# Kernel optimization log

Measured on AMD Instinct MI355X. Metric: run time of the kernel, lower is better.

The kernel has to match this reference:

```python
import jax, jax.numpy as jnp
import numpy as np

NUM_Z = 100   # atomic-number bins hardcoded in the module
G = 512       # number of graphs in the batch (segment count)


def setup_inputs() -> dict:
    key = jax.random.key(0)
    k1, k2, k3 = jax.random.split(key, 3)
    N, D = 50000, 64
    out = jax.random.normal(k1, (N, D), dtype=jnp.float32)
    # atomic numbers in [1, 100], matching the (z-1)*D offset logic
    z_rv = jax.random.randint(k2, (N,), 1, NUM_Z + 1)
    # sorted graph ids in [0, G)
    x_rv_batch = jnp.sort(jax.random.randint(k3, (N,), 0, G))
    return {"out": out, "z_rv": z_rv, "x_rv_batch": x_rv_batch}


def reference(out, z_rv, x_rv_batch):
    # Original math: elem_pool[i, (z_i-1)*D : z_i*D] = out[i] (zeros elsewhere),
    # then global_mean_pool(elem_pool, batch) -> [G, 100*D].
    # Fused form: segment-sum node features into (graph, atomic-number) bins,
    # then divide by per-graph node counts. Identical result, no NxD*100 buffer.
    N, D = out.shape
    keys = x_rv_batch * NUM_Z + (z_rv - 1)                 # [N] combined (graph, bin) id
    sums = jax.ops.segment_sum(out, keys, num_segments=G * NUM_Z)   # [G*100, D]
    counts = jax.ops.segment_sum(jnp.ones((N,), out.dtype), x_rv_batch,
                                 num_segments=G)           # [G] nodes per graph
    pooled = sums.reshape(G, NUM_Z * D) / jnp.maximum(counts, 1.0)[:, None]
    return pooled
```

## Files before the change

### kernel.cpp

```cpp
#include <hip/hip_runtime.h>

#define NUM_Z 100
#define NUM_G 512
#define DIM   64
#define THREADS 1024
#define CHUNK 128

__device__ __forceinline__ int lower_bound_wave(const int* __restrict__ arr, int n,
                                                int target, int lane) {
    int lo = 0, len = n;
    while (len > 0) {
        int step = (len + 63) >> 6;
        int idx  = lo + lane * step;
        int v    = (idx < n) ? arr[idx] : 0x7fffffff;
        unsigned long long m = __ballot(v < target);
        int k = (int)__popcll(m);
        if (k == 0) break;
        int rem = k * step; if (rem > len) rem = len;
        int hi  = lo + rem;
        lo += (k - 1) * step + 1;
        len = hi - lo;
    }
    return lo;
}

__global__ __launch_bounds__(THREADS) void anp_stage_kernel(
    const float4* __restrict__ feat,
    const int*    __restrict__ z,
    const int*    __restrict__ batch,
    float*        __restrict__ pooled,
    int n)
{
    __shared__ float4 tile[CHUNK * 16];
    __shared__ int hist[128];
    __shared__ int scan_tmp[128];
    __shared__ int pref[NUM_Z + 1];
    __shared__ int cursor[NUM_Z];
    __shared__ unsigned short idx_sorted[CHUNK];
    __shared__ int sb[2];
    __shared__ int wtot;

    const int g    = blockIdx.x;
    const int tid  = threadIdx.x;
    const int wave = tid >> 6;
    const int lane = tid & 63;
    const int grp  = tid >> 4;
    const int q    = tid & 15;
    const int b0   = 2 * grp;

    if (tid < 128) hist[tid] = 0;
    if (wave < 2) {
        int r = lower_bound_wave(batch, n, g + wave, lane);
        if (lane == 0) sb[wave] = r;
    }
    __syncthreads();
    const int start = sb[0];
    const int end   = sb[1];
    const int cnt   = end - start;

    float4 a0 = make_float4(0.f, 0.f, 0.f, 0.f);
    float4 a1 = make_float4(0.f, 0.f, 0.f, 0.f);

    const int jrow = tid >> 4;

    for (int cs = start; cs < end; cs += CHUNK) {
        const int m = min(CHUNK, end - cs);

        float4 s0, s1;
        const bool h0 = (jrow      < m);
        const bool h1 = (jrow + 64 < m);
        if (h0) s0 = feat[(size_t)(cs + jrow)      * 16 + q];
        if (h1) s1 = feat[(size_t)(cs + jrow + 64) * 16 + q];

        int zv = 0;
        if (tid < m) {
            zv = z[cs + tid] - 1;
            atomicAdd(&hist[zv], 1);
        }
        __syncthreads();

        if (wave < 2) {
            int e = hist[(wave << 6) + lane];
            #pragma unroll
            for (int d = 1; d < 64; d <<= 1) {
                int t = __shfl_up(e, d, 64);
                if (lane >= d) e += t;
            }
            scan_tmp[(wave << 6) + lane] = e;
            if (wave == 0 && lane == 63) wtot = e;
        }
        __syncthreads();

        if (tid <= NUM_Z) {
            int v = (tid == 0) ? 0
                  : scan_tmp[tid - 1] + ((tid - 1) >= 64 ? wtot : 0);
            pref[tid] = v;
            if (tid < NUM_Z) cursor[tid] = v;
        }
        __syncthreads();

        if (h0) tile[jrow * 16 + q]        = s0;
        if (h1) tile[(jrow + 64) * 16 + q] = s1;
        if (tid < m) {
            int p = atomicAdd(&cursor[zv], 1);
            idx_sorted[p] = (unsigned short)(tid | ((zv & 1) << 15));
        }
        __syncthreads();

        if (grp < 50) {
            const int off = pref[b0];
            const int c   = pref[b0 + 2] - off;
            for (int base = 0; base < c; base += 16) {
                const int nb = min(16, c - base);
                int myraw = (q < nb) ? (int)idx_sorted[off + base + q] : 0;
                #pragma unroll 4
                for (int j = 0; j < nb; ++j) {
                    int raw  = __shfl(myraw, ((lane >> 4) << 4) + j, 64);
                    int nd   = raw & 0x7fff;
                    float pm = (float)(raw >> 15);
                    float4 v = tile[nd * 16 + q];
                    float m0 = 1.0f - pm;
                    a0.x = fmaf(v.x, m0, a0.x); a0.y = fmaf(v.y, m0, a0.y);
                    a0.z = fmaf(v.z, m0, a0.z); a0.w = fmaf(v.w, m0, a0.w);
                    a1.x = fmaf(v.x, pm, a1.x); a1.y = fmaf(v.y, pm, a1.y);
                    a1.z = fmaf(v.z, pm, a1.z); a1.w = fmaf(v.w, pm, a1.w);
                }
            }
        }
        if (cs + CHUNK < end) {
            __syncthreads();
            if (tid < 128) hist[tid] = 0;
            __syncthreads();
        }
    }

    if (grp < 50) {
        const float s = 1.0f / (float)(cnt > 1 ? cnt : 1);
        float4* outv = (float4*)(pooled + (size_t)g * (NUM_Z * DIM));
        outv[(b0 + 0) * 16 + q] = make_float4(a0.x*s, a0.y*s, a0.z*s, a0.w*s);
        outv[(b0 + 1) * 16 + q] = make_float4(a1.x*s, a1.y*s, a1.z*s, a1.w*s);
    }
}

extern "C" void kernel_launch(void* const* d_in, const int* in_sizes, int n_in,
                              void* d_out, int out_size, void* d_ws, size_t ws_size,
                              hipStream_t stream) {
    const float* feat  = (const float*)d_in[0];
    const int*   z     = (const int*)d_in[1];
    const int*   batch = (const int*)d_in[2];
    float* pooled = (float*)d_out;
    const int n = in_sizes[0] / DIM;

    anp_stage_kernel<<<NUM_G, THREADS, 0, stream>>>(
        (const float4*)feat, z, batch, pooled, n);
}
```

Baseline: 11.33 us.

## Locate segment bounds via guessed window scan, prefetch z, merge scan stages

Each block guesses a 2048-element window around its expected segment position, loads batch ids and z values for that window in one coalesced pass, and finds segment start/end with ballot-popcount counts instead of a serial binary search over global memory. If the window does not cover the whole segment, it falls back to the old wave binary search. z values are then read from shared memory, and the two-wave histogram scan collapses into one wave, removing a barrier per chunk. The cost is extra global reads of the window for every block and a dependence on segments being roughly uniform in size.

```diff
diff --git a/kernel.cpp b/kernel.cpp
--- a/kernel.cpp
+++ b/kernel.cpp
@@ -5,6 +5,7 @@
 #define DIM   64
 #define THREADS 1024
 #define CHUNK 128
+#define WIN 2048
 
 __device__ __forceinline__ int lower_bound_wave(const int* __restrict__ arr, int n,
                                                 int target, int lane) {
@@ -24,7 +25,7 @@
     return lo;
 }
 
-__global__ __launch_bounds__(THREADS) void anp_stage_kernel(
+__global__ __launch_bounds__(THREADS) void anp_win_kernel(
     const float4* __restrict__ feat,
     const int*    __restrict__ z,
     const int*    __restrict__ batch,
@@ -32,13 +33,14 @@
     int n)
 {
     __shared__ float4 tile[CHUNK * 16];
+    __shared__ int zwin[WIN];
     __shared__ int hist[128];
-    __shared__ int scan_tmp[128];
     __shared__ int pref[NUM_Z + 1];
     __shared__ int cursor[NUM_Z];
     __shared__ unsigned short idx_sorted[CHUNK];
+    __shared__ int Lpart[16], Epart[16];
+    __shared__ int sbf, sbl;
     __shared__ int sb[2];
-    __shared__ int wtot;
 
     const int g    = blockIdx.x;
     const int tid  = threadIdx.x;
@@ -48,19 +50,55 @@
     const int q    = tid & 15;
     const int b0   = 2 * grp;
 
+    int wbase = (int)(((long long)g * n) / NUM_G) - 960;
+    int wmax  = n - WIN; if (wmax < 0) wmax = 0;
+    if (wbase < 0) wbase = 0;
+    if (wbase > wmax) wbase = wmax;
+
+    const int i0 = wbase + tid, i1 = wbase + tid + THREADS;
+    int bv0 = (i0 < n) ? batch[i0] : 0x7fffffff;
+    int bv1 = (i1 < n) ? batch[i1] : 0x7fffffff;
+    int zv0 = (i0 < n) ? z[i0] : 1;
+    int zv1 = (i1 < n) ? z[i1] : 1;
+
     if (tid < 128) hist[tid] = 0;
-    if (wave < 2) {
-        int r = lower_bound_wave(batch, n, g + wave, lane);
-        if (lane == 0) sb[wave] = r;
+    zwin[tid]           = zv0 - 1;
+    zwin[tid + THREADS] = zv1 - 1;
+    {
+        int l = __popcll(__ballot(bv0 < g))     + __popcll(__ballot(bv1 < g));
+        int e = __popcll(__ballot(bv0 < g + 1)) + __popcll(__ballot(bv1 < g + 1));
+        if (lane == 0) { Lpart[wave] = l; Epart[wave] = e; }
     }
+    if (tid == 0)           sbf = bv0;
+    if (tid == THREADS - 1) sbl = bv1;
     __syncthreads();
-    const int start = sb[0];
-    const int end   = sb[1];
-    const int cnt   = end - start;
+
+    int v = 0;
+    if (lane < 16)      v = Lpart[lane];
+    else if (lane < 32) v = Epart[lane - 16];
+    v += __shfl_xor(v, 1, 64); v += __shfl_xor(v, 2, 64);
+    v += __shfl_xor(v, 4, 64); v += __shfl_xor(v, 8, 64);
+    const int L = __shfl(v, 0, 64);
+    const int E = __shfl(v, 16, 64);
+
+    const bool valid = ((wbase == 0) || (sbf < g)) &&
+                       ((wbase + WIN >= n) || (sbl > g));
+    int start, end;
+    if (valid) {
+        start = wbase + L; end = wbase + E;
+    } else {
+        if (wave < 2) {
+            int r = lower_bound_wave(batch, n, g + wave, lane);
+            if (lane == 0) sb[wave] = r;
+        }
+        __syncthreads();
+        start = sb[0]; end = sb[1];
+    }
+    const int cnt = end - start;
+    const int dlt = start - wbase;
 
     float4 a0 = make_float4(0.f, 0.f, 0.f, 0.f);
     float4 a1 = make_float4(0.f, 0.f, 0.f, 0.f);
-
     const int jrow = tid >> 4;
 
     for (int cs = start; cs < end; cs += CHUNK) {
@@ -72,38 +110,36 @@
         if (h0) s0 = feat[(size_t)(cs + jrow)      * 16 + q];
         if (h1) s1 = feat[(size_t)(cs + jrow + 64) * 16 + q];
 
-        int zv = 0;
+        int zb = 0;
         if (tid < m) {
-            zv = z[cs + tid] - 1;
-            atomicAdd(&hist[zv], 1);
+            zb = valid ? zwin[dlt + (cs - start) + tid] : (z[cs + tid] - 1);
+            atomicAdd(&hist[zb], 1);
         }
         __syncthreads();
 
-        if (wave < 2) {
-            int e = hist[(wave << 6) + lane];
+        if (wave == 0) {
+            int h0v = hist[lane], h1v = hist[64 + lane];
+            int i0v = h0v, i1v = h1v;
             #pragma unroll
             for (int d = 1; d < 64; d <<= 1) {
-                int t = __shfl_up(e, d, 64);
-                if (lane >= d) e += t;
+                int t0 = __shfl_up(i0v, d, 64);
+                int t1 = __shfl_up(i1v, d, 64);
+                if (lane >= d) { i0v += t0; i1v += t1; }
             }
-            scan_tmp[(wave << 6) + lane] = e;
-            if (wave == 0 && lane == 63) wtot = e;
-        }
-        __syncthreads();
-
-        if (tid <= NUM_Z) {
-            int v = (tid == 0) ? 0
-                  : scan_tmp[tid - 1] + ((tid - 1) >= 64 ? wtot : 0);
-            pref[tid] = v;
-            if (tid < NUM_Z) cursor[tid] = v;
+            const int e0 = i0v - h0v, e1 = i1v - h1v;
+            const int tot0 = __shfl(i0v, 63, 64);
+            pref[lane]   = e0;
+            cursor[lane] = e0;
+            if (lane <= 36) pref[64 + lane]   = tot0 + e1;
+            if (lane <= 35) cursor[64 + lane] = tot0 + e1;
         }
         __syncthreads();
 
         if (h0) tile[jrow * 16 + q]        = s0;
         if (h1) tile[(jrow + 64) * 16 + q] = s1;
         if (tid < m) {
-            int p = atomicAdd(&cursor[zv], 1);
-            idx_sorted[p] = (unsigned short)(tid | ((zv & 1) << 15));
+            int p = atomicAdd(&cursor[zb], 1);
+            idx_sorted[p] = (unsigned short)(tid | ((zb & 1) << 15));
         }
         __syncthreads();
 
@@ -118,12 +154,12 @@
                     int raw  = __shfl(myraw, ((lane >> 4) << 4) + j, 64);
                     int nd   = raw & 0x7fff;
                     float pm = (float)(raw >> 15);
-                    float4 v = tile[nd * 16 + q];
+                    float4 vv = tile[nd * 16 + q];
                     float m0 = 1.0f - pm;
-                    a0.x = fmaf(v.x, m0, a0.x); a0.y = fmaf(v.y, m0, a0.y);
-                    a0.z = fmaf(v.z, m0, a0.z); a0.w = fmaf(v.w, m0, a0.w);
-                    a1.x = fmaf(v.x, pm, a1.x); a1.y = fmaf(v.y, pm, a1.y);
-                    a1.z = fmaf(v.z, pm, a1.z); a1.w = fmaf(v.w, pm, a1.w);
+                    a0.x = fmaf(vv.x, m0, a0.x); a0.y = fmaf(vv.y, m0, a0.y);
+                    a0.z = fmaf(vv.z, m0, a0.z); a0.w = fmaf(vv.w, m0, a0.w);
+                    a1.x = fmaf(vv.x, pm, a1.x); a1.y = fmaf(vv.y, pm, a1.y);
+                    a1.z = fmaf(vv.z, pm, a1.z); a1.w = fmaf(vv.w, pm, a1.w);
                 }
             }
         }
@@ -151,6 +187,6 @@
     float* pooled = (float*)d_out;
     const int n = in_sizes[0] / DIM;
 
-    anp_stage_kernel<<<NUM_G, THREADS, 0, stream>>>(
+    anp_win_kernel<<<NUM_G, THREADS, 0, stream>>>(
         (const float4*)feat, z, batch, pooled, n);
 }
```

Measured after the change: 12.14 us. 7.2% more time.
